# Optimization experiments

Hardware: AMD Instinct MI355X
Metric: run time of the kernel (lower is better)

## Reference

```python
import jax, jax.numpy as jnp
import numpy as np

N_NODES = 100000
N_EDGES = 1280000
IN_DIM = 64
OUT_DIM = 64


def setup_inputs() -> dict:
    key = jax.random.key(0)
    k1, k2, k3, k4, k5 = jax.random.split(key, 5)
    features = jax.random.normal(k1, (N_NODES, IN_DIM), dtype=jnp.float32)
    w = jax.random.uniform(k2, (N_EDGES,), dtype=jnp.float32)
    # torch nn.Linear weight is [out, in]; we store it as [in, out] so h @ W
    W = jax.random.normal(k3, (IN_DIM, OUT_DIM), dtype=jnp.float32) * (1.0 / np.sqrt(IN_DIM))
    src = jax.random.randint(k4, (N_EDGES,), 0, N_NODES, dtype=jnp.int64 if jax.config.jax_enable_x64 else jnp.int32)
    dst = jax.random.randint(k5, (N_EDGES,), 0, N_NODES, dtype=jnp.int64 if jax.config.jax_enable_x64 else jnp.int32)
    return {"features": features, "w": w, "W": W, "src": src, "dst": dst}


def reference(features, w, W, src, dst):
    num_nodes = features.shape[0]
    # u_mul_e: per-edge message = h[src] * w  (edge-weighted SpMM gather-multiply)
    msg = features[src] * w[:, None]                     # [E, in_dim]
    # fn.sum('m','h'): scatter-add messages to destination nodes
    agg = jax.ops.segment_sum(msg, dst, num_segments=num_nodes)  # [N, in_dim]
    # D_in = 1 / clamp(in_degree, min=1)
    deg = jax.ops.segment_sum(jnp.ones_like(w), dst, num_segments=num_nodes)
    d_in = 1.0 / jnp.maximum(deg, 1.0)                   # [N]
    h = agg * d_in[:, None]
    # linear (bias=False), activation None, batch_norm False, dropout 0
    return h @ W                                         # [N, out_dim]
```

## Files before the change

### kernel.cpp

```cpp
#include <hip/hip_runtime.h>

#define N_NODES 100000
#define N_EDGES 1280000
#define DIM 64
#define NBINS 391
#define CAP 3712
#define EPB 4096
#define NFB 313
#define CONVB 512
#define NTILES 1563
#define FPAD 68
#define WSCALE (1.0f / 32767.0f)

typedef float floatx4 __attribute__((ext_vector_type(4)));

__device__ __forceinline__ unsigned bf16_rne(float x) {
    unsigned u = __float_as_uint(x);
    return (u + 0x7fffu + ((u >> 16) & 1u)) >> 16;
}
__device__ __forceinline__ float bf_lo(unsigned q) { return __uint_as_float(q << 16); }
__device__ __forceinline__ float bf_hi(unsigned q) { return __uint_as_float(q & 0xffff0000u); }

__global__ __launch_bounds__(256) void k_fill_conv(
    const int* __restrict__ src, const float* __restrict__ w,
    const int* __restrict__ dst, int* __restrict__ cursor,
    uint2* __restrict__ binned,
    const float* __restrict__ feat, const float* __restrict__ W,
    unsigned short* __restrict__ fW) {
    __shared__ union U {
        struct { int h[NBINS]; int base_[NBINS]; } fill;
        struct { float w[DIM * DIM]; float f[64 * FPAD]; } conv;
        __device__ U() {}
    } sm;
    int t = threadIdx.x;

    if (blockIdx.x < NFB) {
        for (int i = t; i < NBINS; i += 256) sm.fill.h[i] = 0;
        __syncthreads();
        int eb = blockIdx.x * EPB;
        int d[16], sv[16];
        unsigned wq[16];
        #pragma unroll
        for (int j = 0; j < 16; ++j) {
            int e = eb + j * 256 + t;
            if (e < N_EDGES) {
                d[j] = dst[e];
                sv[j] = src[e];
                wq[j] = (unsigned)(w[e] * 32767.0f + 0.5f);
                atomicAdd(&sm.fill.h[d[j] >> 8], 1);
            } else d[j] = -1;
        }
        __syncthreads();
        for (int i = t; i < NBINS; i += 256) {
            int c = sm.fill.h[i];
            sm.fill.base_[i] = c ? atomicAdd(&cursor[i], c) : 0;
            sm.fill.h[i] = 0;
        }
        __syncthreads();
        #pragma unroll
        for (int j = 0; j < 16; ++j) {
            if (d[j] >= 0) {
                int bin = d[j] >> 8;
                int pos = sm.fill.base_[bin] + atomicAdd(&sm.fill.h[bin], 1);
                binned[bin * CAP + pos] =
                    make_uint2((unsigned)sv[j] | ((unsigned)(d[j] & 255) << 17), wq[j]);
            }
        }
    } else {
        #pragma unroll
        for (int i = 0; i < DIM * DIM / 256; ++i)
            sm.conv.w[t + i * 256] = W[t + i * 256];
        const float4* lds_w4 = (const float4*)sm.conv.w;
        float4* lds_f4 = (float4*)sm.conv.f;
        int tx = t & 15, ny = t >> 4;
        int rr = t >> 2, seg = t & 3;

        for (int tb = blockIdx.x - NFB; tb < NTILES; tb += CONVB) {
            int nb = tb * 64;
            __syncthreads();
            #pragma unroll
            for (int q = 0; q < 4; ++q) {
                float4 v = (nb + rr < N_NODES)
                           ? ((const float4*)feat)[(size_t)(nb + rr) * 16 + seg * 4 + q]
                           : make_float4(0.f, 0.f, 0.f, 0.f);
                lds_f4[(rr * FPAD + seg * 16 + q * 4) >> 2] = v;
            }
            __syncthreads();
            float acc[4][4];
            #pragma unroll
            for (int i = 0; i < 4; ++i)
                #pragma unroll
                for (int j = 0; j < 4; ++j) acc[i][j] = 0.f;
            for (int k0 = 0; k0 < DIM; k0 += 4) {
                float4 hv[4], wv[4];
                #pragma unroll
                for (int i = 0; i < 4; ++i)
                    hv[i] = lds_f4[((ny * 4 + i) * FPAD + k0) >> 2];
                #pragma unroll
                for (int j = 0; j < 4; ++j)
                    wv[j] = lds_w4[((k0 + j) * DIM + tx * 4) >> 2];
                #pragma unroll
                for (int i = 0; i < 4; ++i) {
                    const float* hp = (const float*)&hv[i];
                    #pragma unroll
                    for (int kk = 0; kk < 4; ++kk) {
                        float hk = hp[kk];
                        acc[i][0] = fmaf(hk, ((const float*)&wv[kk])[0], acc[i][0]);
                        acc[i][1] = fmaf(hk, ((const float*)&wv[kk])[1], acc[i][1]);
                        acc[i][2] = fmaf(hk, ((const float*)&wv[kk])[2], acc[i][2]);
                        acc[i][3] = fmaf(hk, ((const float*)&wv[kk])[3], acc[i][3]);
                    }
                }
            }
            #pragma unroll
            for (int i = 0; i < 4; ++i) {
                int node = nb + ny * 4 + i;
                if (node < N_NODES) {
                    ushort4 o;
                    o.x = (unsigned short)bf16_rne(acc[i][0]);
                    o.y = (unsigned short)bf16_rne(acc[i][1]);
                    o.z = (unsigned short)bf16_rne(acc[i][2]);
                    o.w = (unsigned short)bf16_rne(acc[i][3]);
                    *(ushort4*)(fW + (size_t)node * DIM + tx * 4) = o;
                }
            }
        }
    }
}

__global__ __launch_bounds__(512) void k_sortbin(const uint2* __restrict__ binned,
                                                 const int* __restrict__ cursor,
                                                 unsigned* __restrict__ csrp,
                                                 int2* __restrict__ noff) {
    __shared__ int h[256];
    __shared__ int excl[256];
    __shared__ unsigned stage[CAP];
    int b = blockIdx.x, t = threadIdx.x;
    int total = cursor[b];
    int segbase = b * CAP;
    if (t < 256) h[t] = 0;
    __syncthreads();
    for (int i = t; i < total; i += 512)
        atomicAdd(&h[(binned[segbase + i].x >> 17) & 255], 1);
    __syncthreads();
    int v = 0;
    if (t < 256) { v = h[t]; excl[t] = v; }
    __syncthreads();
    for (int off = 1; off < 256; off <<= 1) {
        int add = 0;
        if (t < 256 && t >= off) add = excl[t - off];
        __syncthreads();
        if (t < 256) excl[t] += add;
        __syncthreads();
    }
    if (t < 256) {
        int ex = excl[t] - v;
        excl[t] = ex;
        int node = (b << 8) + t;
        if (node < N_NODES) noff[node] = make_int2(segbase + ex, v);
        h[t] = 0;
    }
    __syncthreads();
    for (int i = t; i < total; i += 512) {
        uint2 e = binned[segbase + i];
        int o = (e.x >> 17) & 255;
        int pos = excl[o] + atomicAdd(&h[o], 1);
        if (pos < CAP) stage[pos] = (e.x & 0x1ffffu) | (e.y << 17);
    }
    __syncthreads();
    for (int i = t; i < total; i += 512)
        csrp[segbase + i] = stage[i];
}

__global__ __launch_bounds__(256) void k_gather(const uint4* __restrict__ fW4,
                                                const unsigned* __restrict__ csrp,
                                                const int2* __restrict__ noff,
                                                float* __restrict__ out) {
    int lane = threadIdx.x & 63;
    int h = lane >> 5;
    int g2 = (lane >> 3) & 3;
    int s = lane & 7;
    int wave = (blockIdx.x * 256 + threadIdx.x) >> 6;
    int nw = gridDim.x * 4;

    for (int pair = wave; pair < N_NODES / 2; pair += nw) {
        int node = pair * 2 + h;
        int2 oc = noff[node];
        int start = oc.x, c = oc.y;
        int end = start + c;
        float a[8] = {0, 0, 0, 0, 0, 0, 0, 0};
        for (int i = start; i < end; i += 16) {
            int i0 = i + g2, i1 = i + 4 + g2, i2 = i + 8 + g2, i3 = i + 12 + g2;
            unsigned p0 = __builtin_nontemporal_load(csrp + ((i0 < end) ? i0 : start));
            unsigned p1 = __builtin_nontemporal_load(csrp + ((i1 < end) ? i1 : start));
            unsigned p2 = __builtin_nontemporal_load(csrp + ((i2 < end) ? i2 : start));
            unsigned p3 = __builtin_nontemporal_load(csrp + ((i3 < end) ? i3 : start));
            float w0 = (i0 < end) ? (float)(p0 >> 17) * WSCALE : 0.f;
            float w1 = (i1 < end) ? (float)(p1 >> 17) * WSCALE : 0.f;
            float w2 = (i2 < end) ? (float)(p2 >> 17) * WSCALE : 0.f;
            float w3 = (i3 < end) ? (float)(p3 >> 17) * WSCALE : 0.f;
            uint4 q0 = fW4[((size_t)(p0 & 0x1ffffu) << 3) + s];
            uint4 q1 = fW4[((size_t)(p1 & 0x1ffffu) << 3) + s];
            uint4 q2 = fW4[((size_t)(p2 & 0x1ffffu) << 3) + s];
            uint4 q3 = fW4[((size_t)(p3 & 0x1ffffu) << 3) + s];
            a[0] = fmaf(bf_lo(q0.x), w0, a[0]); a[1] = fmaf(bf_hi(q0.x), w0, a[1]);
            a[2] = fmaf(bf_lo(q0.y), w0, a[2]); a[3] = fmaf(bf_hi(q0.y), w0, a[3]);
            a[4] = fmaf(bf_lo(q0.z), w0, a[4]); a[5] = fmaf(bf_hi(q0.z), w0, a[5]);
            a[6] = fmaf(bf_lo(q0.w), w0, a[6]); a[7] = fmaf(bf_hi(q0.w), w0, a[7]);
            a[0] = fmaf(bf_lo(q1.x), w1, a[0]); a[1] = fmaf(bf_hi(q1.x), w1, a[1]);
            a[2] = fmaf(bf_lo(q1.y), w1, a[2]); a[3] = fmaf(bf_hi(q1.y), w1, a[3]);
            a[4] = fmaf(bf_lo(q1.z), w1, a[4]); a[5] = fmaf(bf_hi(q1.z), w1, a[5]);
            a[6] = fmaf(bf_lo(q1.w), w1, a[6]); a[7] = fmaf(bf_hi(q1.w), w1, a[7]);
            a[0] = fmaf(bf_lo(q2.x), w2, a[0]); a[1] = fmaf(bf_hi(q2.x), w2, a[1]);
            a[2] = fmaf(bf_lo(q2.y), w2, a[2]); a[3] = fmaf(bf_hi(q2.y), w2, a[3]);
            a[4] = fmaf(bf_lo(q2.z), w2, a[4]); a[5] = fmaf(bf_hi(q2.z), w2, a[5]);
            a[6] = fmaf(bf_lo(q2.w), w2, a[6]); a[7] = fmaf(bf_hi(q2.w), w2, a[7]);
            a[0] = fmaf(bf_lo(q3.x), w3, a[0]); a[1] = fmaf(bf_hi(q3.x), w3, a[1]);
            a[2] = fmaf(bf_lo(q3.y), w3, a[2]); a[3] = fmaf(bf_hi(q3.y), w3, a[3]);
            a[4] = fmaf(bf_lo(q3.z), w3, a[4]); a[5] = fmaf(bf_hi(q3.z), w3, a[5]);
            a[6] = fmaf(bf_lo(q3.w), w3, a[6]); a[7] = fmaf(bf_hi(q3.w), w3, a[7]);
        }
        #pragma unroll
        for (int j = 0; j < 8; ++j) {
            a[j] += __shfl_xor(a[j], 8, 64);
            a[j] += __shfl_xor(a[j], 16, 64);
        }
        float dinv = 1.0f / fmaxf((float)c, 1.0f);
        if (g2 == 0) {
            floatx4 o0, o1;
            o0.x = a[0] * dinv; o0.y = a[1] * dinv; o0.z = a[2] * dinv; o0.w = a[3] * dinv;
            o1.x = a[4] * dinv; o1.y = a[5] * dinv; o1.z = a[6] * dinv; o1.w = a[7] * dinv;
            floatx4* op = (floatx4*)out + (size_t)node * 16 + s * 2;
            __builtin_nontemporal_store(o0, op + 0);
            __builtin_nontemporal_store(o1, op + 1);
        }
    }
}

extern "C" void kernel_launch(void* const* d_in, const int* in_sizes, int n_in,
                              void* d_out, int out_size, void* d_ws, size_t ws_size,
                              hipStream_t stream) {
    const float* feat = (const float*)d_in[0];
    const float* w    = (const float*)d_in[1];
    const float* W    = (const float*)d_in[2];
    const int*   src  = (const int*)d_in[3];
    const int*   dst  = (const int*)d_in[4];
    float* out = (float*)d_out;

    unsigned short* fW = (unsigned short*)d_ws;
    uint2* binned  = (uint2*)(fW + (size_t)N_NODES * DIM);
    unsigned* csrp = (unsigned*)(binned + (size_t)NBINS * CAP);
    int2* noff     = (int2*)(csrp + (size_t)NBINS * CAP);
    int* cursor    = (int*)(noff + N_NODES);

    hipMemsetAsync(cursor, 0, NBINS * sizeof(int), stream);

    k_fill_conv<<<NFB + CONVB, 256, 0, stream>>>(src, w, dst, cursor, binned,
                                                 feat, W, fW);
    k_sortbin<<<NBINS, 512, 0, stream>>>(binned, cursor, csrp, noff);
    k_gather<<<4096, 256, 0, stream>>>((const uint4*)fW, csrp, noff, out);
}
```

Measured before the change: 142.9 us.

## Move feature-weight GEMM into sort kernel and halve bin size

The dense features@W conversion blocks move out of the edge-binning kernel and now run alongside the per-bin counting-sort blocks in a single 512-thread launch. Bins shrink from 256 to 128 destination nodes, doubling the bin count and cutting per-bin capacity and shared staging. The goal is to overlap the compute-bound GEMM with the latency-bound sort and to give the sort more, smaller blocks for better occupancy. The trade-off is that the fill kernel now runs alone, and the GEMM tile mapping changes to 2 rows per thread for 512 threads.

```diff
diff --git a/kernel.cpp b/kernel.cpp
--- a/kernel.cpp
+++ b/kernel.cpp
@@ -3,8 +3,9 @@
 #define N_NODES 100000
 #define N_EDGES 1280000
 #define DIM 64
-#define NBINS 391
-#define CAP 3712
+#define NBINS 782
+#define BINN 128
+#define CAP 1984
 #define EPB 4096
 #define NFB 313
 #define CONVB 512
@@ -21,86 +22,129 @@
 __device__ __forceinline__ float bf_lo(unsigned q) { return __uint_as_float(q << 16); }
 __device__ __forceinline__ float bf_hi(unsigned q) { return __uint_as_float(q & 0xffff0000u); }
 
-__global__ __launch_bounds__(256) void k_fill_conv(
+__global__ __launch_bounds__(256) void k_fill(
     const int* __restrict__ src, const float* __restrict__ w,
     const int* __restrict__ dst, int* __restrict__ cursor,
-    uint2* __restrict__ binned,
+    uint2* __restrict__ binned) {
+    __shared__ int h[NBINS];
+    __shared__ int base_[NBINS];
+    int t = threadIdx.x;
+    for (int i = t; i < NBINS; i += 256) h[i] = 0;
+    __syncthreads();
+    int eb = blockIdx.x * EPB;
+    int d[16], sv[16];
+    unsigned wq[16];
+    #pragma unroll
+    for (int j = 0; j < 16; ++j) {
+        int e = eb + j * 256 + t;
+        if (e < N_EDGES) {
+            d[j] = dst[e];
+            sv[j] = src[e];
+            wq[j] = (unsigned)(w[e] * 32767.0f + 0.5f);
+            atomicAdd(&h[d[j] >> 7], 1);
+        } else d[j] = -1;
+    }
+    __syncthreads();
+    for (int i = t; i < NBINS; i += 256) {
+        int c = h[i];
+        base_[i] = c ? atomicAdd(&cursor[i], c) : 0;
+        h[i] = 0;
+    }
+    __syncthreads();
+    #pragma unroll
+    for (int j = 0; j < 16; ++j) {
+        if (d[j] >= 0) {
+            int bin = d[j] >> 7;
+            int pos = base_[bin] + atomicAdd(&h[bin], 1);
+            binned[bin * CAP + pos] =
+                make_uint2((unsigned)sv[j] | ((unsigned)(d[j] & 127) << 17), wq[j]);
+        }
+    }
+}
+
+__global__ __launch_bounds__(512) void k_sortconv(
+    const uint2* __restrict__ binned, const int* __restrict__ cursor,
+    unsigned* __restrict__ csrp, int2* __restrict__ noff,
     const float* __restrict__ feat, const float* __restrict__ W,
     unsigned short* __restrict__ fW) {
     __shared__ union U {
-        struct { int h[NBINS]; int base_[NBINS]; } fill;
+        struct { int h[BINN]; int excl[BINN]; unsigned stage[CAP]; } so;
         struct { float w[DIM * DIM]; float f[64 * FPAD]; } conv;
         __device__ U() {}
     } sm;
     int t = threadIdx.x;
 
-    if (blockIdx.x < NFB) {
-        for (int i = t; i < NBINS; i += 256) sm.fill.h[i] = 0;
-        __syncthreads();
-        int eb = blockIdx.x * EPB;
-        int d[16], sv[16];
-        unsigned wq[16];
-        #pragma unroll
-        for (int j = 0; j < 16; ++j) {
-            int e = eb + j * 256 + t;
-            if (e < N_EDGES) {
-                d[j] = dst[e];
-                sv[j] = src[e];
-                wq[j] = (unsigned)(w[e] * 32767.0f + 0.5f);
-                atomicAdd(&sm.fill.h[d[j] >> 8], 1);
-            } else d[j] = -1;
-        }
-        __syncthreads();
-        for (int i = t; i < NBINS; i += 256) {
-            int c = sm.fill.h[i];
-            sm.fill.base_[i] = c ? atomicAdd(&cursor[i], c) : 0;
-            sm.fill.h[i] = 0;
-        }
-        __syncthreads();
-        #pragma unroll
-        for (int j = 0; j < 16; ++j) {
-            if (d[j] >= 0) {
-                int bin = d[j] >> 8;
-                int pos = sm.fill.base_[bin] + atomicAdd(&sm.fill.h[bin], 1);
-                binned[bin * CAP + pos] =
-                    make_uint2((unsigned)sv[j] | ((unsigned)(d[j] & 255) << 17), wq[j]);
-            }
-        }
+    if (blockIdx.x < NBINS) {
+        int b = blockIdx.x;
+        int total = cursor[b];
+        int segbase = b * CAP;
+        if (t < BINN) sm.so.h[t] = 0;
+        __syncthreads();
+        for (int i = t; i < total; i += 512)
+            atomicAdd(&sm.so.h[(binned[segbase + i].x >> 17) & 127], 1);
+        __syncthreads();
+        int v = 0;
+        if (t < BINN) { v = sm.so.h[t]; sm.so.excl[t] = v; }
+        __syncthreads();
+        for (int off = 1; off < BINN; off <<= 1) {
+            int add = 0;
+            if (t < BINN && t >= off) add = sm.so.excl[t - off];
+            __syncthreads();
+            if (t < BINN) sm.so.excl[t] += add;
+            __syncthreads();
+        }
+        if (t < BINN) {
+            int ex = sm.so.excl[t] - v;
+            sm.so.excl[t] = ex;
+            int node = (b << 7) + t;
+            if (node < N_NODES) noff[node] = make_int2(segbase + ex, v);
+            sm.so.h[t] = 0;
+        }
+        __syncthreads();
+        for (int i = t; i < total; i += 512) {
+            uint2 e = binned[segbase + i];
+            int o = (e.x >> 17) & 127;
+            int pos = sm.so.excl[o] + atomicAdd(&sm.so.h[o], 1);
+            if (pos < CAP) sm.so.stage[pos] = (e.x & 0x1ffffu) | (e.y << 17);
+        }
+        __syncthreads();
+        for (int i = t; i < total; i += 512)
+            csrp[segbase + i] = sm.so.stage[i];
     } else {
         #pragma unroll
-        for (int i = 0; i < DIM * DIM / 256; ++i)
-            sm.conv.w[t + i * 256] = W[t + i * 256];
+        for (int i = 0; i < DIM * DIM / 512; ++i)
+            sm.conv.w[t + i * 512] = W[t + i * 512];
         const float4* lds_w4 = (const float4*)sm.conv.w;
         float4* lds_f4 = (float4*)sm.conv.f;
         int tx = t & 15, ny = t >> 4;
-        int rr = t >> 2, seg = t & 3;
-
-        for (int tb = blockIdx.x - NFB; tb < NTILES; tb += CONVB) {
+        int rr = t >> 3, seg = t & 7;
+
+        for (int tb = blockIdx.x - NBINS; tb < NTILES; tb += CONVB) {
             int nb = tb * 64;
             __syncthreads();
             #pragma unroll
-            for (int q = 0; q < 4; ++q) {
+            for (int q = 0; q < 2; ++q) {
                 float4 v = (nb + rr < N_NODES)
-                           ? ((const float4*)feat)[(size_t)(nb + rr) * 16 + seg * 4 + q]
+                           ? ((const float4*)feat)[(size_t)(nb + rr) * 16 + seg * 2 + q]
                            : make_float4(0.f, 0.f, 0.f, 0.f);
-                lds_f4[(rr * FPAD + seg * 16 + q * 4) >> 2] = v;
+                lds_f4[(rr * FPAD + seg * 8 + q * 4) >> 2] = v;
             }
             __syncthreads();
-            float acc[4][4];
+            float acc[2][4];
             #pragma unroll
-            for (int i = 0; i < 4; ++i)
+            for (int i = 0; i < 2; ++i)
                 #pragma unroll
                 for (int j = 0; j < 4; ++j) acc[i][j] = 0.f;
             for (int k0 = 0; k0 < DIM; k0 += 4) {
-                float4 hv[4], wv[4];
-                #pragma unroll
-                for (int i = 0; i < 4; ++i)
-                    hv[i] = lds_f4[((ny * 4 + i) * FPAD + k0) >> 2];
+                float4 hv[2], wv[4];
+                #pragma unroll
+                for (int i = 0; i < 2; ++i)
+                    hv[i] = lds_f4[((ny * 2 + i) * FPAD + k0) >> 2];
                 #pragma unroll
                 for (int j = 0; j < 4; ++j)
                     wv[j] = lds_w4[((k0 + j) * DIM + tx * 4) >> 2];
                 #pragma unroll
-                for (int i = 0; i < 4; ++i) {
+                for (int i = 0; i < 2; ++i) {
                     const float* hp = (const float*)&hv[i];
                     #pragma unroll
                     for (int kk = 0; kk < 4; ++kk) {
@@ -113,8 +157,8 @@
                 }
             }
             #pragma unroll
-            for (int i = 0; i < 4; ++i) {
-                int node = nb + ny * 4 + i;
+            for (int i = 0; i < 2; ++i) {
+                int node = nb + ny * 2 + i;
                 if (node < N_NODES) {
                     ushort4 o;
                     o.x = (unsigned short)bf16_rne(acc[i][0]);
@@ -126,50 +170,6 @@
             }
         }
     }
-}
-
-__global__ __launch_bounds__(512) void k_sortbin(const uint2* __restrict__ binned,
-                                                 const int* __restrict__ cursor,
-                                                 unsigned* __restrict__ csrp,
-                                                 int2* __restrict__ noff) {
-    __shared__ int h[256];
-    __shared__ int excl[256];
-    __shared__ unsigned stage[CAP];
-    int b = blockIdx.x, t = threadIdx.x;
-    int total = cursor[b];
-    int segbase = b * CAP;
-    if (t < 256) h[t] = 0;
-    __syncthreads();
-    for (int i = t; i < total; i += 512)
-        atomicAdd(&h[(binned[segbase + i].x >> 17) & 255], 1);
-    __syncthreads();
-    int v = 0;
-    if (t < 256) { v = h[t]; excl[t] = v; }
-    __syncthreads();
-    for (int off = 1; off < 256; off <<= 1) {
-        int add = 0;
-        if (t < 256 && t >= off) add = excl[t - off];
-        __syncthreads();
-        if (t < 256) excl[t] += add;
-        __syncthreads();
-    }
-    if (t < 256) {
-        int ex = excl[t] - v;
-        excl[t] = ex;
-        int node = (b << 8) + t;
-        if (node < N_NODES) noff[node] = make_int2(segbase + ex, v);
-        h[t] = 0;
-    }
-    __syncthreads();
-    for (int i = t; i < total; i += 512) {
-        uint2 e = binned[segbase + i];
-        int o = (e.x >> 17) & 255;
-        int pos = excl[o] + atomicAdd(&h[o], 1);
-        if (pos < CAP) stage[pos] = (e.x & 0x1ffffu) | (e.y << 17);
-    }
-    __syncthreads();
-    for (int i = t; i < total; i += 512)
-        csrp[segbase + i] = stage[i];
 }
 
 __global__ __launch_bounds__(256) void k_gather(const uint4* __restrict__ fW4,
@@ -255,8 +255,8 @@
 
     hipMemsetAsync(cursor, 0, NBINS * sizeof(int), stream);
 
-    k_fill_conv<<<NFB + CONVB, 256, 0, stream>>>(src, w, dst, cursor, binned,
-                                                 feat, W, fW);
-    k_sortbin<<<NBINS, 512, 0, stream>>>(binned, cursor, csrp, noff);
+    k_fill<<<NFB, 256, 0, stream>>>(src, w, dst, cursor, binned);
+    k_sortconv<<<NBINS + CONVB, 512, 0, stream>>>(binned, cursor, csrp, noff,
+                                                  feat, W, fW);
     k_gather<<<4096, 256, 0, stream>>>((const uint4*)fW, csrp, noff, out);
 }
```

New measurement: 319.1 us. 2.23x slower.

## Halve bin width to 128 nodes and keep binned edges in registers during sort

Applied to the files above, without the earlier changes.

Destination bins shrink from 256 to 128 nodes, which doubles the bin count and roughly halves the per-bin capacity. The per-bin sort now loads each thread's up to four edges into registers once and reuses them for both the histogram and the scatter, instead of reading global memory twice. More, smaller sort blocks should raise parallelism and cut LDS use. The risks are more cursor atomics in the fill stage, and overflow if a bin exceeds 1984 entries, since the bounds check on stage writes was removed.

```diff
diff --git a/kernel.cpp b/kernel.cpp
--- a/kernel.cpp
+++ b/kernel.cpp
@@ -3,8 +3,9 @@
 #define N_NODES 100000
 #define N_EDGES 1280000
 #define DIM 64
-#define NBINS 391
-#define CAP 3712
+#define NBINS 782
+#define BINN 128
+#define CAP 1984
 #define EPB 4096
 #define NFB 313
 #define CONVB 512
@@ -47,7 +48,7 @@
                 d[j] = dst[e];
                 sv[j] = src[e];
                 wq[j] = (unsigned)(w[e] * 32767.0f + 0.5f);
-                atomicAdd(&sm.fill.h[d[j] >> 8], 1);
+                atomicAdd(&sm.fill.h[d[j] >> 7], 1);
             } else d[j] = -1;
         }
         __syncthreads();
@@ -60,10 +61,10 @@
         #pragma unroll
         for (int j = 0; j < 16; ++j) {
             if (d[j] >= 0) {
-                int bin = d[j] >> 8;
+                int bin = d[j] >> 7;
                 int pos = sm.fill.base_[bin] + atomicAdd(&sm.fill.h[bin], 1);
                 binned[bin * CAP + pos] =
-                    make_uint2((unsigned)sv[j] | ((unsigned)(d[j] & 255) << 17), wq[j]);
+                    make_uint2((unsigned)sv[j] | ((unsigned)(d[j] & 127) << 17), wq[j]);
             }
         }
     } else {
@@ -132,42 +133,52 @@
                                                  const int* __restrict__ cursor,
                                                  unsigned* __restrict__ csrp,
                                                  int2* __restrict__ noff) {
-    __shared__ int h[256];
-    __shared__ int excl[256];
+    __shared__ int h[BINN];
+    __shared__ int excl[BINN];
     __shared__ unsigned stage[CAP];
     int b = blockIdx.x, t = threadIdx.x;
     int total = cursor[b];
     int segbase = b * CAP;
-    if (t < 256) h[t] = 0;
-    __syncthreads();
-    for (int i = t; i < total; i += 512)
-        atomicAdd(&h[(binned[segbase + i].x >> 17) & 255], 1);
-    __syncthreads();
+    if (t < BINN) h[t] = 0;
+    __syncthreads();
+
+    int i0 = t, i1 = t + 512, i2 = t + 1024, i3 = t + 1536;
+    uint2 e0 = make_uint2(0, 0), e1 = e0, e2 = e0, e3 = e0;
+    if (i0 < total) { e0 = binned[segbase + i0]; atomicAdd(&h[(e0.x >> 17) & 127], 1); }
+    if (i1 < total) { e1 = binned[segbase + i1]; atomicAdd(&h[(e1.x >> 17) & 127], 1); }
+    if (i2 < total) { e2 = binned[segbase + i2]; atomicAdd(&h[(e2.x >> 17) & 127], 1); }
+    if (i3 < total) { e3 = binned[segbase + i3]; atomicAdd(&h[(e3.x >> 17) & 127], 1); }
+    __syncthreads();
+
     int v = 0;
-    if (t < 256) { v = h[t]; excl[t] = v; }
-    __syncthreads();
-    for (int off = 1; off < 256; off <<= 1) {
+    if (t < BINN) { v = h[t]; excl[t] = v; }
+    __syncthreads();
+    for (int off = 1; off < BINN; off <<= 1) {
         int add = 0;
-        if (t < 256 && t >= off) add = excl[t - off];
-        __syncthreads();
-        if (t < 256) excl[t] += add;
-        __syncthreads();
-    }
-    if (t < 256) {
+        if (t < BINN && t >= off) add = excl[t - off];
+        __syncthreads();
+        if (t < BINN) excl[t] += add;
+        __syncthreads();
+    }
+    if (t < BINN) {
         int ex = excl[t] - v;
         excl[t] = ex;
-        int node = (b << 8) + t;
+        int node = (b << 7) + t;
         if (node < N_NODES) noff[node] = make_int2(segbase + ex, v);
         h[t] = 0;
     }
     __syncthreads();
-    for (int i = t; i < total; i += 512) {
-        uint2 e = binned[segbase + i];
-        int o = (e.x >> 17) & 255;
-        int pos = excl[o] + atomicAdd(&h[o], 1);
-        if (pos < CAP) stage[pos] = (e.x & 0x1ffffu) | (e.y << 17);
-    }
-    __syncthreads();
+
+    if (i0 < total) { int o = (e0.x >> 17) & 127; int p = excl[o] + atomicAdd(&h[o], 1);
+                      stage[p] = (e0.x & 0x1ffffu) | (e0.y << 17); }
+    if (i1 < total) { int o = (e1.x >> 17) & 127; int p = excl[o] + atomicAdd(&h[o], 1);
+                      stage[p] = (e1.x & 0x1ffffu) | (e1.y << 17); }
+    if (i2 < total) { int o = (e2.x >> 17) & 127; int p = excl[o] + atomicAdd(&h[o], 1);
+                      stage[p] = (e2.x & 0x1ffffu) | (e2.y << 17); }
+    if (i3 < total) { int o = (e3.x >> 17) & 127; int p = excl[o] + atomicAdd(&h[o], 1);
+                      stage[p] = (e3.x & 0x1ffffu) | (e3.y << 17); }
+    __syncthreads();
+
     for (int i = t; i < total; i += 512)
         csrp[segbase + i] = stage[i];
 }
```

New measurement: 144.8 us. Within noise of the previous version (+1.3%).
